# Kernel optimization log

Measured on AMD Instinct MI355X. Metric: run time of the kernel, lower is better.

The kernel has to match this reference:

```python
import jax, jax.numpy as jnp
import numpy as np

EPS = 1e-05


def setup_inputs() -> dict:
    key = jax.random.key(0)
    x = jax.random.normal(key, (256, 256, 256), dtype=jnp.float32)
    return {"x": x}


def reference(x):
    # x: [B, N, N] dependency score logits
    B, N, _ = x.shape
    eye = jnp.eye(N, dtype=x.dtype)
    exp_x = jnp.exp(x)                                  # [B, N, N]
    diag_exp = jnp.exp(jnp.diagonal(x, axis1=-2, axis2=-1))  # [B, N] root scores

    # Build Laplacian: zero diagonal, negate off-diagonals, column sums on diag
    lap = (exp_x + EPS) * (1.0 - eye)                   # masked_fill diag with 0
    colsum = lap.sum(axis=-2)                           # torch sum(0) = column sums
    lap = -lap + colsum[:, None, :] * eye               # -lap + diag(colsum)
    # Replace row 0 with exp of the diagonal of input (root selection row)
    lap = lap.at[:, 0, :].set(diag_exp)

    inv = jnp.linalg.inv(lap)                           # batched inverse [B, N, N]
    d = jnp.diagonal(inv, axis1=-2, axis2=-1)           # [B, N]

    term1 = exp_x * d[:, None, :]                       # factor[i,j] = inv_diag[j]
    term2 = exp_x * jnp.swapaxes(inv, -1, -2)
    term1 = term1.at[:, :, 0].set(0.0)
    term2 = term2.at[:, 0, :].set(0.0)
    out = term1 - term2

    roots = diag_exp * inv[:, :, 0]                     # inv.T[0] == inv[:, 0]
    out = out + eye * roots[:, :, None]                 # add diag(roots)
    return out
```

## Files before the change

### kernel.cpp

```cpp
#include <hip/hip_runtime.h>
#include <math.h>

#define N 256
#define BS 32
#define NB_ 8
#define EPS 1e-5f

__global__ __launch_bounds__(1024, 4) void mtt_fused(const float* __restrict__ x,
                                                     float* __restrict__ out) {
    constexpr int LDR = N + 8;
    __shared__ alignas(16) float  Rf[BS][LDR];
    __shared__ alignas(16) float  CfT[BS][LDR];
    __shared__ float  Pf[BS][BS + 1];
    __shared__ double dsum[4][N];
    __shared__ float  sdx[N];
    __shared__ float  sdiag_f[N];
    __shared__ float  sroot_f[N];
    __shared__ int    indx[BS];

    const int tid = threadIdx.x;
    const int ty = tid >> 5, tx = tid & 31;
    const int R0  = ty << 3;
    const int c0a = tx << 2;
    const int c0b = 128 + (tx << 2);
    const float* xb = x + (size_t)blockIdx.x * N * N;
    float* ob = out + (size_t)blockIdx.x * N * N;

    float m[8][8];

    double csacc = 0.0;
    const int tq = tid >> 8, jc = tid & 255;
#pragma unroll 1
    for (int s = 0; s < 8; ++s) {
        {
            const int rl = tid >> 5, cl = (tid & 31) << 3;
            const float* src = &xb[(size_t)(32 * s + rl) * N + cl];
            *(float4*)&Rf[rl][cl]     = *(const float4*)&src[0];
            *(float4*)&Rf[rl][cl + 4] = *(const float4*)&src[4];
        }
        __syncthreads();
#pragma unroll
        for (int r = 0; r < 8; ++r)
            csacc += (double)expf(Rf[(tq << 3) + r][jc]);
        if (tid < 32) sdx[32 * s + tid] = expf(Rf[tid][32 * s + tid]);
        if ((tx >> 3) == s) {
            const int jb = (tx & 7) << 2;
#pragma unroll
            for (int cc = 0; cc < 4; ++cc)
#pragma unroll
                for (int r = 0; r < 8; ++r)
                    m[r][cc] = -(expf(Rf[jb + cc][R0 + r]) + EPS);
        }
        if (s >= 4 && (tx >> 3) == s - 4) {
            const int jb = (tx & 7) << 2;
#pragma unroll
            for (int cc = 0; cc < 4; ++cc)
#pragma unroll
                for (int r = 0; r < 8; ++r)
                    m[r][4 + cc] = -(expf(Rf[jb + cc][R0 + r]) + EPS);
        }
        __syncthreads();
    }
    dsum[tq][jc] = csacc;
    __syncthreads();
    if (tid < N)
        dsum[0][tid] = dsum[0][tid] + dsum[1][tid] + dsum[2][tid] + dsum[3][tid];
    __syncthreads();
    if (ty < 16) {
#pragma unroll
        for (int r = 0; r < 8; ++r) {
            const int i = R0 + r;
            if (tx == ((ty << 1) + (r >> 2)) && i != 0)
                m[r][r & 3] =
                    (float)(dsum[0][i] - (double)sdx[i] + 255.0 * (double)EPS);
        }
    } else {
#pragma unroll
        for (int r = 0; r < 8; ++r) {
            const int i = R0 + r;
            if (tx == (((ty - 16) << 1) + (r >> 2)))
                m[r][4 + (r & 3)] =
                    (float)(dsum[0][i] - (double)sdx[i] + 255.0 * (double)EPS);
        }
    }
    if (tx == 0) {
#pragma unroll
        for (int r = 0; r < 8; ++r) m[r][0] = sdx[R0 + r];
    }

#pragma unroll 1
    for (int kb = 0; kb < NB_; ++kb) {
        const int k0 = kb * BS;
        const bool rowOwner = (ty >> 2) == kb;
        const bool h0piv = (kb < 4) && ((tx >> 3) == kb);
        const bool h1piv = (kb >= 4) && ((tx >> 3) == kb - 4);
        const int lr = (ty & 3) << 3;
        const int lc = (tx & 7) << 2;

        if (rowOwner) {
#pragma unroll
            for (int r = 0; r < 8; ++r) {
                *(float4*)&Rf[lr + r][c0a] =
                    make_float4(m[r][0], m[r][1], m[r][2], m[r][3]);
                *(float4*)&Rf[lr + r][c0b] =
                    make_float4(m[r][4], m[r][5], m[r][6], m[r][7]);
            }
        }
        if (h0piv) {
#pragma unroll
            for (int cc = 0; cc < 4; ++cc) {
                *(float4*)&CfT[lc + cc][R0] =
                    make_float4(m[0][cc], m[1][cc], m[2][cc], m[3][cc]);
                *(float4*)&CfT[lc + cc][R0 + 4] =
                    make_float4(m[4][cc], m[5][cc], m[6][cc], m[7][cc]);
            }
        }
        if (h1piv) {
#pragma unroll
            for (int cc = 0; cc < 4; ++cc) {
                *(float4*)&CfT[lc + cc][R0] =
                    make_float4(m[0][4 + cc], m[1][4 + cc], m[2][4 + cc], m[3][4 + cc]);
                *(float4*)&CfT[lc + cc][R0 + 4] =
                    make_float4(m[4][4 + cc], m[5][4 + cc], m[6][4 + cc], m[7][4 + cc]);
            }
        }
        __syncthreads();

        if (tid < 64) {
            const int l = tid;
            const int row = l & 31;
            const int h = l >> 5, hb = h << 5;
            double p[16];
#pragma unroll
            for (int j = 0; j < 16; ++j)
                p[j] = (double)CfT[(h << 4) + j][k0 + row];

#pragma unroll
            for (int k2 = 0; k2 < BS; ++k2) {
                const int hk2 = k2 >> 4, jk2 = k2 & 15;
                const double cand = p[jk2];
                double av = (h == hk2 && row >= k2) ? fabs(cand) : -1.0;
                double vv = cand;
                int idx = row;
#pragma unroll
                for (int off = 1; off < 64; off <<= 1) {
                    const double oav = __shfl_xor(av, off);
                    const double ovv = __shfl_xor(vv, off);
                    const int    oi  = __shfl_xor(idx, off);
                    if (oav > av || (oav == av && oi < idx)) { av = oav; vv = ovv; idx = oi; }
                }
                const double pivinv = 1.0 / vv;
                if (l == 0) indx[k2] = idx;
                const int prt = (row == k2) ? idx : ((row == idx) ? k2 : row);
                const int sl2 = prt + hb;
#pragma unroll
                for (int j = 0; j < 16; ++j) p[j] = __shfl(p[j], sl2);
                const double scol = __shfl(p[jk2], row + (hk2 << 5));
                const int pl = k2 + hb;
                const bool isPivRow = (row == k2);
#pragma unroll
                for (int j = 0; j < 16; ++j) {
                    const double prow = __shfl(p[j], pl);
                    const bool isK2col = (h == hk2) && (j == jk2);
                    const double srw  = isK2col ? pivinv : prow * pivinv;
                    const double base = isK2col ? 0.0 : p[j];
                    p[j] = isPivRow ? srw : fma(-scol, srw, base);
                }
            }
#pragma unroll
            for (int j = 0; j < 16; ++j)
                Pf[row][(h << 4) + j] = (float)p[j];
            if (l < 32) {
#pragma unroll 1
                for (int k2 = BS - 1; k2 >= 0; --k2) {
                    const int pp = indx[k2];
                    if (pp != k2) {
                        const float t = Pf[l][k2];
                        Pf[l][k2] = Pf[l][pp];
                        Pf[l][pp] = t;
                    }
                }
            }
        }
        __syncthreads();

        {
            float a0[8];
#pragma unroll
            for (int c = 0; c < 8; ++c) a0[c] = 0.f;
#pragma unroll 2
            for (int mm = 0; mm < BS; ++mm) {
                const float p0 = Pf[ty][mm];
                const float4 r0 = *(const float4*)&Rf[mm][c0a];
                const float4 r1 = *(const float4*)&Rf[mm][c0b];
                a0[0] = fmaf(p0, r0.x, a0[0]);
                a0[1] = fmaf(p0, r0.y, a0[1]);
                a0[2] = fmaf(p0, r0.z, a0[2]);
                a0[3] = fmaf(p0, r0.w, a0[3]);
                a0[4] = fmaf(p0, r1.x, a0[4]);
                a0[5] = fmaf(p0, r1.y, a0[5]);
                a0[6] = fmaf(p0, r1.z, a0[6]);
                a0[7] = fmaf(p0, r1.w, a0[7]);
            }
            if (h0piv) {
#pragma unroll
                for (int cc = 0; cc < 4; ++cc) a0[cc] = Pf[ty][lc + cc];
            }
            if (h1piv) {
#pragma unroll
                for (int cc = 0; cc < 4; ++cc) a0[4 + cc] = Pf[ty][lc + cc];
            }
            __syncthreads();
            *(float4*)&Rf[ty][c0a] = make_float4(a0[0], a0[1], a0[2], a0[3]);
            *(float4*)&Rf[ty][c0b] = make_float4(a0[4], a0[5], a0[6], a0[7]);
        }
        __syncthreads();

        if (rowOwner) {
#pragma unroll
            for (int r = 0; r < 8; ++r) {
                const float4 b0 = *(const float4*)&Rf[lr + r][c0a];
                const float4 b1 = *(const float4*)&Rf[lr + r][c0b];
                m[r][0] = b0.x; m[r][1] = b0.y; m[r][2] = b0.z; m[r][3] = b0.w;
                m[r][4] = b1.x; m[r][5] = b1.y; m[r][6] = b1.z; m[r][7] = b1.w;
            }
        } else {
            if (h0piv) {
#pragma unroll
                for (int r = 0; r < 8; ++r) {
                    m[r][0] = 0.f; m[r][1] = 0.f; m[r][2] = 0.f; m[r][3] = 0.f;
                }
            }
            if (h1piv) {
#pragma unroll
                for (int r = 0; r < 8; ++r) {
                    m[r][4] = 0.f; m[r][5] = 0.f; m[r][6] = 0.f; m[r][7] = 0.f;
                }
            }
#pragma unroll 2
            for (int mm = 0; mm < BS; ++mm) {
                const float4 rv0 = *(const float4*)&Rf[mm][c0a];
                const float4 rv1 = *(const float4*)&Rf[mm][c0b];
                const float4 cv0 = *(const float4*)&CfT[mm][R0];
                const float4 cv1 = *(const float4*)&CfT[mm][R0 + 4];
                const float cc8[8] = {cv0.x, cv0.y, cv0.z, cv0.w,
                                      cv1.x, cv1.y, cv1.z, cv1.w};
#pragma unroll
                for (int r = 0; r < 8; ++r) {
                    const float cr = -cc8[r];
                    m[r][0] = fmaf(cr, rv0.x, m[r][0]);
                    m[r][1] = fmaf(cr, rv0.y, m[r][1]);
                    m[r][2] = fmaf(cr, rv0.z, m[r][2]);
                    m[r][3] = fmaf(cr, rv0.w, m[r][3]);
                    m[r][4] = fmaf(cr, rv1.x, m[r][4]);
                    m[r][5] = fmaf(cr, rv1.y, m[r][5]);
                    m[r][6] = fmaf(cr, rv1.z, m[r][6]);
                    m[r][7] = fmaf(cr, rv1.w, m[r][7]);
                }
            }
        }
        __syncthreads();
    }

    if (ty < 16) {
#pragma unroll
        for (int r = 0; r < 8; ++r) {
            const int i = R0 + r;
            if (tx == ((ty << 1) + (r >> 2))) sdiag_f[i] = m[r][r & 3];
        }
    } else {
#pragma unroll
        for (int r = 0; r < 8; ++r) {
            const int i = R0 + r;
            if (tx == (((ty - 16) << 1) + (r >> 2))) sdiag_f[i] = m[r][4 + (r & 3)];
        }
    }
    if (ty == 0) {
        *(float4*)&sroot_f[c0a] = make_float4(m[0][0], m[0][1], m[0][2], m[0][3]);
        *(float4*)&sroot_f[c0b] = make_float4(m[0][4], m[0][5], m[0][6], m[0][7]);
    }
    __syncthreads();

#pragma unroll
    for (int r = 0; r < 8; ++r) {
        const int a = R0 + r;
        const float rt = sroot_f[a];
        {
            const float4 x0 = *(const float4*)&xb[(size_t)a * N + c0a];
            float ov[4];
#pragma unroll
            for (int c = 0; c < 4; ++c) {
                const int b_ = c0a + c;
                const float e = expf((c == 0) ? x0.x : (c == 1) ? x0.y
                                    : (c == 2) ? x0.z : x0.w);
                float o = (b_ == 0) ? 0.0f : e * sdiag_f[b_];
                if (a != 0) o -= e * m[r][c];
                if (a == b_) o += e * rt;
                ov[c] = o;
            }
            *(float4*)&ob[(size_t)a * N + c0a] = make_float4(ov[0], ov[1], ov[2], ov[3]);
        }
        {
            const float4 x1 = *(const float4*)&xb[(size_t)a * N + c0b];
            float ov[4];
#pragma unroll
            for (int c = 0; c < 4; ++c) {
                const int b_ = c0b + c;
                const float e = expf((c == 0) ? x1.x : (c == 1) ? x1.y
                                    : (c == 2) ? x1.z : x1.w);
                float o = e * sdiag_f[b_];
                if (a != 0) o -= e * m[r][4 + c];
                if (a == b_) o += e * rt;
                ov[c] = o;
            }
            *(float4*)&ob[(size_t)a * N + c0b] = make_float4(ov[0], ov[1], ov[2], ov[3]);
        }
    }
}

extern "C" void kernel_launch(void* const* d_in, const int* in_sizes, int n_in,
                              void* d_out, int out_size, void* d_ws, size_t ws_size,
                              hipStream_t stream) {
    const float* x = (const float*)d_in[0];
    float* out = (float*)d_out;
    mtt_fused<<<256, 1024, 0, stream>>>(x, out);
}
```

Measured before the change: 509.3 us.

## Look ahead: invert next pivot block during trailing update with double-buffered row panels

```diff
diff --git a/kernel.cpp b/kernel.cpp
--- a/kernel.cpp
+++ b/kernel.cpp
@@ -9,9 +9,11 @@
 __global__ __launch_bounds__(1024, 4) void mtt_fused(const float* __restrict__ x,
                                                      float* __restrict__ out) {
     constexpr int LDR = N + 8;
-    __shared__ alignas(16) float  Rf[BS][LDR];
+    __shared__ alignas(16) float  RfA[BS][LDR];
+    __shared__ alignas(16) float  RfB[BS][LDR];
     __shared__ alignas(16) float  CfT[BS][LDR];
     __shared__ float  Pf[BS][BS + 1];
+    __shared__ float  Psn[BS][BS + 1];
     __shared__ double dsum[4][N];
     __shared__ float  sdx[N];
     __shared__ float  sdiag_f[N];
@@ -35,21 +37,21 @@
         {
             const int rl = tid >> 5, cl = (tid & 31) << 3;
             const float* src = &xb[(size_t)(32 * s + rl) * N + cl];
-            *(float4*)&Rf[rl][cl]     = *(const float4*)&src[0];
-            *(float4*)&Rf[rl][cl + 4] = *(const float4*)&src[4];
+            *(float4*)&RfA[rl][cl]     = *(const float4*)&src[0];
+            *(float4*)&RfA[rl][cl + 4] = *(const float4*)&src[4];
         }
         __syncthreads();
 #pragma unroll
         for (int r = 0; r < 8; ++r)
-            csacc += (double)expf(Rf[(tq << 3) + r][jc]);
-        if (tid < 32) sdx[32 * s + tid] = expf(Rf[tid][32 * s + tid]);
+            csacc += (double)expf(RfA[(tq << 3) + r][jc]);
+        if (tid < 32) sdx[32 * s + tid] = expf(RfA[tid][32 * s + tid]);
         if ((tx >> 3) == s) {
             const int jb = (tx & 7) << 2;
 #pragma unroll
             for (int cc = 0; cc < 4; ++cc)
 #pragma unroll
                 for (int r = 0; r < 8; ++r)
-                    m[r][cc] = -(expf(Rf[jb + cc][R0 + r]) + EPS);
+                    m[r][cc] = -(expf(RfA[jb + cc][R0 + r]) + EPS);
         }
         if (s >= 4 && (tx >> 3) == s - 4) {
             const int jb = (tx & 7) << 2;
@@ -57,7 +59,7 @@
             for (int cc = 0; cc < 4; ++cc)
 #pragma unroll
                 for (int r = 0; r < 8; ++r)
-                    m[r][4 + cc] = -(expf(Rf[jb + cc][R0 + r]) + EPS);
+                    m[r][4 + cc] = -(expf(RfA[jb + cc][R0 + r]) + EPS);
         }
         __syncthreads();
     }
@@ -88,100 +90,140 @@
         for (int r = 0; r < 8; ++r) m[r][0] = sdx[R0 + r];
     }
 
+#define STAGE_PANELS(kb_)                                                      \
+    do {                                                                       \
+        const bool rO = (ty >> 2) == (kb_);                                    \
+        const bool p0 = ((kb_) < 4) && ((tx >> 3) == (kb_));                   \
+        const bool p1 = ((kb_) >= 4) && ((tx >> 3) == (kb_) - 4);              \
+        const int lr_ = (ty & 3) << 3, lc_ = (tx & 7) << 2;                    \
+        if (rO) {                                                              \
+            for (int r = 0; r < 8; ++r) {                                      \
+                *(float4*)&RfA[lr_ + r][c0a] =                                 \
+                    make_float4(m[r][0], m[r][1], m[r][2], m[r][3]);           \
+                *(float4*)&RfA[lr_ + r][c0b] =                                 \
+                    make_float4(m[r][4], m[r][5], m[r][6], m[r][7]);           \
+            }                                                                  \
+        }                                                                      \
+        if (p0) {                                                              \
+            for (int cc = 0; cc < 4; ++cc) {                                   \
+                *(float4*)&CfT[lc_ + cc][R0] =                                 \
+                    make_float4(m[0][cc], m[1][cc], m[2][cc], m[3][cc]);       \
+                *(float4*)&CfT[lc_ + cc][R0 + 4] =                             \
+                    make_float4(m[4][cc], m[5][cc], m[6][cc], m[7][cc]);       \
+            }                                                                  \
+        }                                                                      \
+        if (p1) {                                                              \
+            for (int cc = 0; cc < 4; ++cc) {                                   \
+                *(float4*)&CfT[lc_ + cc][R0] =                                 \
+                    make_float4(m[0][4+cc], m[1][4+cc], m[2][4+cc], m[3][4+cc]); \
+                *(float4*)&CfT[lc_ + cc][R0 + 4] =                             \
+                    make_float4(m[4][4+cc], m[5][4+cc], m[6][4+cc], m[7][4+cc]); \
+            }                                                                  \
+        }                                                                      \
+    } while (0)
+
+#define STAGE_PSN(kbn_)                                                        \
+    do {                                                                       \
+        const bool rO = (ty >> 2) == (kbn_);                                   \
+        const int lr_ = (ty & 3) << 3, lc_ = (tx & 7) << 2;                    \
+        if (rO && (kbn_) < 4 && ((tx >> 3) == (kbn_))) {                       \
+            for (int r = 0; r < 8; ++r)                                        \
+                for (int cc = 0; cc < 4; ++cc)                                 \
+                    Psn[lr_ + r][lc_ + cc] = m[r][cc];                         \
+        }                                                                      \
+        if (rO && (kbn_) >= 4 && ((tx >> 3) == (kbn_) - 4)) {                  \
+            for (int r = 0; r < 8; ++r)                                        \
+                for (int cc = 0; cc < 4; ++cc)                                 \
+                    Psn[lr_ + r][lc_ + cc] = m[r][4 + cc];                     \
+        }                                                                      \
+    } while (0)
+
+#define INVERT_PSN(PARKBUF)                                                    \
+    do {                                                                       \
+        float* park = &PARKBUF[0][0];                                          \
+        for (int r = 0; r < 8; ++r) {                                          \
+            *(float4*)&park[tid * 66 + (r << 3)] =                             \
+                make_float4(m[r][0], m[r][1], m[r][2], m[r][3]);               \
+            *(float4*)&park[tid * 66 + (r << 3) + 4] =                         \
+                make_float4(m[r][4], m[r][5], m[r][6], m[r][7]);               \
+        }                                                                      \
+        asm volatile("" ::: "memory");                                         \
+        {                                                                      \
+            const int l = tid;                                                 \
+            const int row = l & 31;                                            \
+            const int h = l >> 5, hb = h << 5;                                 \
+            double p[16];                                                      \
+            for (int j = 0; j < 16; ++j)                                       \
+                p[j] = (double)Psn[row][(h << 4) + j];                         \
+            for (int k2 = 0; k2 < BS; ++k2) {                                  \
+                const int hk2 = k2 >> 4, jk2 = k2 & 15;                        \
+                const double cand = p[jk2];                                    \
+                double av = (h == hk2 && row >= k2) ? fabs(cand) : -1.0;       \
+                double vv = cand;                                              \
+                int idx = row;                                                 \
+                for (int off = 1; off < 64; off <<= 1) {                       \
+                    const double oav = __shfl_xor(av, off);                    \
+                    const double ovv = __shfl_xor(vv, off);                    \
+                    const int    oi  = __shfl_xor(idx, off);                   \
+                    if (oav > av || (oav == av && oi < idx)) {                 \
+                        av = oav; vv = ovv; idx = oi;                          \
+                    }                                                          \
+                }                                                              \
+                const double pivinv = 1.0 / vv;                                \
+                if (l == 0) indx[k2] = idx;                                    \
+                const int prt = (row == k2) ? idx : ((row == idx) ? k2 : row); \
+                const int sl2 = prt + hb;                                      \
+                for (int j = 0; j < 16; ++j) p[j] = __shfl(p[j], sl2);         \
+                const double scol = __shfl(p[jk2], row + (hk2 << 5));          \
+                const int pl = k2 + hb;                                        \
+                const bool isPivRow = (row == k2);                             \
+                for (int j = 0; j < 16; ++j) {                                 \
+                    const double prow = __shfl(p[j], pl);                      \
+                    const bool isK2col = (h == hk2) && (j == jk2);             \
+                    const double srw  = isK2col ? pivinv : prow * pivinv;      \
+                    const double base = isK2col ? 0.0 : p[j];                  \
+                    p[j] = isPivRow ? srw : fma(-scol, srw, base);             \
+                }                                                              \
+            }                                                                  \
+            for (int j = 0; j < 16; ++j)                                       \
+                Pf[row][(h << 4) + j] = (float)p[j];                           \
+            if (l < 32) {                                                      \
+                for (int k2 = BS - 1; k2 >= 0; --k2) {                         \
+                    const int pp = indx[k2];                                   \
+                    if (pp != k2) {                                            \
+                        const float t = Pf[l][k2];                             \
+                        Pf[l][k2] = Pf[l][pp];                                 \
+                        Pf[l][pp] = t;                                         \
+                    }                                                          \
+                }                                                              \
+            }                                                                  \
+        }                                                                      \
+        asm volatile("" ::: "memory");                                         \
+        for (int r = 0; r < 8; ++r) {                                          \
+            const float4 q0 = *(const float4*)&park[tid * 66 + (r << 3)];      \
+            const float4 q1 = *(const float4*)&park[tid * 66 + (r << 3) + 4];  \
+            m[r][0] = q0.x; m[r][1] = q0.y; m[r][2] = q0.z; m[r][3] = q0.w;    \
+            m[r][4] = q1.x; m[r][5] = q1.y; m[r][6] = q1.z; m[r][7] = q1.w;    \
+        }                                                                      \
+    } while (0)
+
+    STAGE_PANELS(0);
+    STAGE_PSN(0);
+    __syncthreads();
+    if (tid < 64) INVERT_PSN(RfB);
+    __syncthreads();
+
 #pragma unroll 1
     for (int kb = 0; kb < NB_; ++kb) {
-        const int k0 = kb * BS;
         const bool rowOwner = (ty >> 2) == kb;
         const bool h0piv = (kb < 4) && ((tx >> 3) == kb);
         const bool h1piv = (kb >= 4) && ((tx >> 3) == kb - 4);
         const int lr = (ty & 3) << 3;
         const int lc = (tx & 7) << 2;
-
-        if (rowOwner) {
-#pragma unroll
-            for (int r = 0; r < 8; ++r) {
-                *(float4*)&Rf[lr + r][c0a] =
-                    make_float4(m[r][0], m[r][1], m[r][2], m[r][3]);
-                *(float4*)&Rf[lr + r][c0b] =
-                    make_float4(m[r][4], m[r][5], m[r][6], m[r][7]);
-            }
-        }
-        if (h0piv) {
-#pragma unroll
-            for (int cc = 0; cc < 4; ++cc) {
-                *(float4*)&CfT[lc + cc][R0] =
-                    make_float4(m[0][cc], m[1][cc], m[2][cc], m[3][cc]);
-                *(float4*)&CfT[lc + cc][R0 + 4] =
-                    make_float4(m[4][cc], m[5][cc], m[6][cc], m[7][cc]);
-            }
-        }
-        if (h1piv) {
-#pragma unroll
-            for (int cc = 0; cc < 4; ++cc) {
-                *(float4*)&CfT[lc + cc][R0] =
-                    make_float4(m[0][4 + cc], m[1][4 + cc], m[2][4 + cc], m[3][4 + cc]);
-                *(float4*)&CfT[lc + cc][R0 + 4] =
-                    make_float4(m[4][4 + cc], m[5][4 + cc], m[6][4 + cc], m[7][4 + cc]);
-            }
-        }
-        __syncthreads();
-
-        if (tid < 64) {
-            const int l = tid;
-            const int row = l & 31;
-            const int h = l >> 5, hb = h << 5;
-            double p[16];
-#pragma unroll
-            for (int j = 0; j < 16; ++j)
-                p[j] = (double)CfT[(h << 4) + j][k0 + row];
-
-#pragma unroll
-            for (int k2 = 0; k2 < BS; ++k2) {
-                const int hk2 = k2 >> 4, jk2 = k2 & 15;
-                const double cand = p[jk2];
-                double av = (h == hk2 && row >= k2) ? fabs(cand) : -1.0;
-                double vv = cand;
-                int idx = row;
-#pragma unroll
-                for (int off = 1; off < 64; off <<= 1) {
-                    const double oav = __shfl_xor(av, off);
-                    const double ovv = __shfl_xor(vv, off);
-                    const int    oi  = __shfl_xor(idx, off);
-                    if (oav > av || (oav == av && oi < idx)) { av = oav; vv = ovv; idx = oi; }
-                }
-                const double pivinv = 1.0 / vv;
-                if (l == 0) indx[k2] = idx;
-                const int prt = (row == k2) ? idx : ((row == idx) ? k2 : row);
-                const int sl2 = prt + hb;
-#pragma unroll
-                for (int j = 0; j < 16; ++j) p[j] = __shfl(p[j], sl2);
-                const double scol = __shfl(p[jk2], row + (hk2 << 5));
-                const int pl = k2 + hb;
-                const bool isPivRow = (row == k2);
-#pragma unroll
-                for (int j = 0; j < 16; ++j) {
-                    const double prow = __shfl(p[j], pl);
-                    const bool isK2col = (h == hk2) && (j == jk2);
-                    const double srw  = isK2col ? pivinv : prow * pivinv;
-                    const double base = isK2col ? 0.0 : p[j];
-                    p[j] = isPivRow ? srw : fma(-scol, srw, base);
-                }
-            }
-#pragma unroll
-            for (int j = 0; j < 16; ++j)
-                Pf[row][(h << 4) + j] = (float)p[j];
-            if (l < 32) {
-#pragma unroll 1
-                for (int k2 = BS - 1; k2 >= 0; --k2) {
-                    const int pp = indx[k2];
-                    if (pp != k2) {
-                        const float t = Pf[l][k2];
-                        Pf[l][k2] = Pf[l][pp];
-                        Pf[l][pp] = t;
-                    }
-                }
-            }
-        }
+        const int kn0 = (kb + 1) << 5;
+
+        if (kb > 0) STAGE_PANELS(kb);
+        if (kb < 7) STAGE_PSN(kb + 1);
         __syncthreads();
 
         {
@@ -191,8 +233,8 @@
 #pragma unroll 2
             for (int mm = 0; mm < BS; ++mm) {
                 const float p0 = Pf[ty][mm];
-                const float4 r0 = *(const float4*)&Rf[mm][c0a];
-                const float4 r1 = *(const float4*)&Rf[mm][c0b];
+                const float4 r0 = *(const float4*)&RfA[mm][c0a];
+                const float4 r1 = *(const float4*)&RfA[mm][c0b];
                 a0[0] = fmaf(p0, r0.x, a0[0]);
                 a0[1] = fmaf(p0, r0.y, a0[1]);
                 a0[2] = fmaf(p0, r0.z, a0[2]);
@@ -210,17 +252,28 @@
 #pragma unroll
                 for (int cc = 0; cc < 4; ++cc) a0[4 + cc] = Pf[ty][lc + cc];
             }
-            __syncthreads();
-            *(float4*)&Rf[ty][c0a] = make_float4(a0[0], a0[1], a0[2], a0[3]);
-            *(float4*)&Rf[ty][c0b] = make_float4(a0[4], a0[5], a0[6], a0[7]);
-        }
-        __syncthreads();
+            *(float4*)&RfB[ty][c0a] = make_float4(a0[0], a0[1], a0[2], a0[3]);
+            *(float4*)&RfB[ty][c0b] = make_float4(a0[4], a0[5], a0[6], a0[7]);
+        }
+        __syncthreads();
+
+        if (kb < 7) {
+            const int i = ty, j = tx;
+            float acc = Psn[i][j];
+#pragma unroll 4
+            for (int mm = 0; mm < BS; ++mm)
+                acc = fmaf(-CfT[mm][kn0 + i], RfB[mm][kn0 + j], acc);
+            Psn[i][j] = acc;
+        }
+        __syncthreads();
+
+        if (kb < 7 && tid < 64) INVERT_PSN(RfA);
 
         if (rowOwner) {
 #pragma unroll
             for (int r = 0; r < 8; ++r) {
-                const float4 b0 = *(const float4*)&Rf[lr + r][c0a];
-                const float4 b1 = *(const float4*)&Rf[lr + r][c0b];
+                const float4 b0 = *(const float4*)&RfB[lr + r][c0a];
+                const float4 b1 = *(const float4*)&RfB[lr + r][c0b];
                 m[r][0] = b0.x; m[r][1] = b0.y; m[r][2] = b0.z; m[r][3] = b0.w;
                 m[r][4] = b1.x; m[r][5] = b1.y; m[r][6] = b1.z; m[r][7] = b1.w;
             }
@@ -239,8 +292,8 @@
             }
 #pragma unroll 2
             for (int mm = 0; mm < BS; ++mm) {
-                const float4 rv0 = *(const float4*)&Rf[mm][c0a];
-                const float4 rv1 = *(const float4*)&Rf[mm][c0b];
+                const float4 rv0 = *(const float4*)&RfB[mm][c0a];
+                const float4 rv1 = *(const float4*)&RfB[mm][c0b];
                 const float4 cv0 = *(const float4*)&CfT[mm][R0];
                 const float4 cv1 = *(const float4*)&CfT[mm][R0 + 4];
                 const float cc8[8] = {cv0.x, cv0.y, cv0.z, cv0.w,
```

After: 519.7 us. +2.0%, slower.
